# Kernel tuning notes

Measured on AMD Instinct MI355X. Metric: run time of the kernel, lower is better.

## Reference

```python
import jax, jax.numpy as jnp
import numpy as np

B, T, D = 8, 2048, 256
EPS_NORM = 1e-8
EPS_LN = 1e-6


def _layer_norm(x, gamma, beta):
    mu = jnp.mean(x, axis=-1, keepdims=True)
    var = jnp.var(x, axis=-1, keepdims=True)
    return (x - mu) * jax.lax.rsqrt(var + EPS_LN) * gamma + beta


def setup_inputs() -> dict:
    key = jax.random.key(0)
    ks = jax.random.split(key, 8)
    xav = np.sqrt(2.0 / (D + D)).astype(np.float32)  # xavier_uniform-ish scale
    a_fea = jax.random.normal(ks[0], (B, T, D), jnp.float32)
    v_fea = jax.random.normal(ks[1], (B, T, D), jnp.float32)
    Wv1 = jax.random.normal(ks[2], (D, D), jnp.float32) * xav
    Wv2 = jax.random.normal(ks[3], (D, D), jnp.float32) * xav
    Wa1 = jax.random.normal(ks[4], (D, D), jnp.float32) * xav
    Wa2 = jax.random.normal(ks[5], (D, D), jnp.float32) * xav
    ln_gamma = jnp.ones((D,), jnp.float32)
    ln_beta = jnp.zeros((D,), jnp.float32)
    thr_val = jnp.asarray(0.099, jnp.float32)
    return {"a_fea": a_fea, "v_fea": v_fea, "Wv1": Wv1, "Wv2": Wv2,
            "Wa1": Wa1, "Wa2": Wa2, "ln_gamma": ln_gamma, "ln_beta": ln_beta,
            "thr_val": thr_val}


def reference(a_fea, v_fea, Wv1, Wv2, Wa1, Wa2, ln_gamma, ln_beta, thr_val):
    # Dropout is identity in eval mode. Linear(bias=False): x @ W^T; here W is [in, out].
    v_b1 = jax.nn.relu(jnp.einsum('btd,dh->bth', v_fea, Wv1))
    v_b2 = jax.nn.relu(jnp.einsum('btd,dh->bth', v_fea, Wv2))
    a_b1 = jax.nn.relu(jnp.einsum('btd,dh->bth', a_fea, Wa1))
    a_b2 = jax.nn.relu(jnp.einsum('btd,dh->bth', a_fea, Wa2))

    scale = 1.0 / jnp.sqrt(jnp.asarray(v_b2.shape[2], jnp.float32))
    # relu-gated cross-modal scores [B, Tv, Ta]
    beta = jax.nn.relu(jnp.einsum('bvh,bah->bva', v_b2, a_b1) * scale)

    # v->a: normalize over audio axis, threshold-sparsify
    beta_va = beta / (jnp.sum(beta, axis=-1, keepdims=True) + EPS_NORM)
    gamma_va = jnp.where(beta_va > thr_val, beta_va, 0.0)
    # a->v: transpose of UN-normalized beta (faithful to source ordering)
    beta_av = jnp.swapaxes(beta, 1, 2)
    beta_av = beta_av / (jnp.sum(beta_av, axis=-1, keepdims=True) + EPS_NORM)
    gamma_av = jnp.where(beta_av > thr_val, beta_av, 0.0)

    a_pos = jnp.einsum('bva,bah->bvh', gamma_va, a_b2)
    v_pos = jnp.einsum('bav,bvh->bah', gamma_av, v_b1)

    v_psp = _layer_norm(v_fea + a_pos, ln_gamma, ln_beta)
    a_psp = _layer_norm(a_fea + v_pos, ln_gamma, ln_beta)
    return (v_psp + a_psp) * 0.5
```

## Files before the change

kernel.cpp:

```cpp
#include <hip/hip_runtime.h>
#include <stdint.h>

#define B_ 8
#define T_ 2048
#define D_ 256
#define M_ (B_*T_)

typedef uint16_t u16;
typedef __attribute__((ext_vector_type(8))) short   short8;
typedef __attribute__((ext_vector_type(8))) __bf16  bf16x8;
typedef __attribute__((ext_vector_type(4))) float   f32x4;
typedef __attribute__((ext_vector_type(4))) uint32_t u32x4;

__device__ __forceinline__ float bf2f(u16 b){
    union { uint32_t u; float f; } v; v.u = ((uint32_t)b) << 16; return v.f;
}
__device__ __forceinline__ u16 f2bf(float f){
    union { float f; uint32_t u; } v; v.f = f;
    uint32_t u = v.u;
    u += 0x7FFFu + ((u >> 16) & 1u);
    return (u16)(u >> 16);
}

typedef __attribute__((address_space(1))) void gvoid;
typedef __attribute__((address_space(3))) void lvoid;
__device__ __forceinline__ void gl16(const void* g, void* l){
    __builtin_amdgcn_global_load_lds((gvoid*)(unsigned long long)g, (lvoid*)l, 16, 0, 0);
}

__global__ void k_detect(const uint32_t* g, int* flag){
    *flag = (g[0] == 0x3F803F80u) ? 0 : 1;
}

struct WtArgs { const void* w[4]; u16* wt[4]; const int* flag; };

__global__ __launch_bounds__(256) void k_wt(WtArgs a){
    int f32in = *a.flag;
    int m = blockIdx.y;
    int d = blockIdx.x;
    int h = threadIdx.x;
    float val;
    if (f32in) val = ((const float*)a.w[m])[(size_t)d * D_ + h];
    else       val = bf2f(((const u16*)a.w[m])[(size_t)d * D_ + h]);
    a.wt[m][(size_t)h * D_ + d] = f2bf(val);
}

struct ProjArgs { const void* x[4]; const u16* wt[4]; u16* y[4]; u16* yt[4]; const int* flag; };

__global__ __launch_bounds__(256) void k_proj(ProjArgs args){
    __shared__ __align__(16) u16 Xs[128][72];
    __shared__ __align__(16) u16 Ws[128][72];
    int f32in = *args.flag;
    int id = blockIdx.x;
    int m  = id & 127;
    int vh = id >> 7;
    int hh = vh & 1;
    int v  = vh >> 1;
    const u16* Wt = args.wt[v];
    u16*       Y  = args.y[v];
    u16*       YT = args.yt[v];
    int t_base = m * 128;
    int h_base = hh * 128;

    int tid  = threadIdx.x;
    int w    = tid >> 6, lane = tid & 63;
    int wm   = w >> 1, wn = w & 1;
    int l15  = lane & 15, quad = lane >> 4;

    int srow = tid >> 1;
    int shalf = tid & 1;

    f32x4 acc[4][4];
#pragma unroll
    for (int i = 0; i < 4; ++i)
#pragma unroll
        for (int j = 0; j < 4; ++j) acc[i][j] = (f32x4){0.f,0.f,0.f,0.f};

    float4 pXf[8];
    short8 pXb[4];
    short8 pW[4];

    const float* Xf = (const float*)args.x[v] + (size_t)(t_base + srow)*D_ + shalf*32;
    const u16*   Xb = (const u16*)args.x[v]   + (size_t)(t_base + srow)*D_ + shalf*32;
    const u16*   Wp = Wt + (size_t)(h_base + srow)*D_ + shalf*32;

    if (f32in){
#pragma unroll
        for (int i = 0; i < 8; ++i) pXf[i] = *(const float4*)(Xf + i*4);
    } else {
#pragma unroll
        for (int i = 0; i < 4; ++i) pXb[i] = *(const short8*)(Xb + i*8);
    }
#pragma unroll
    for (int i = 0; i < 4; ++i) pW[i] = *(const short8*)(Wp + i*8);

    for (int k0 = 0; k0 < D_; k0 += 64){
        __syncthreads();
        if (f32in){
#pragma unroll
            for (int i = 0; i < 4; ++i){
                float4 a0 = pXf[i*2], a1 = pXf[i*2+1];
                short8 o;
                o[0]=(short)f2bf(a0.x); o[1]=(short)f2bf(a0.y); o[2]=(short)f2bf(a0.z); o[3]=(short)f2bf(a0.w);
                o[4]=(short)f2bf(a1.x); o[5]=(short)f2bf(a1.y); o[6]=(short)f2bf(a1.z); o[7]=(short)f2bf(a1.w);
                *(short8*)(&Xs[srow][shalf*32 + i*8]) = o;
            }
        } else {
#pragma unroll
            for (int i = 0; i < 4; ++i) *(short8*)(&Xs[srow][shalf*32 + i*8]) = pXb[i];
        }
#pragma unroll
        for (int i = 0; i < 4; ++i) *(short8*)(&Ws[srow][shalf*32 + i*8]) = pW[i];

        int kn = k0 + 64;
        if (kn < D_){
            if (f32in){
#pragma unroll
                for (int i = 0; i < 8; ++i) pXf[i] = *(const float4*)(Xf + kn + i*4);
            } else {
#pragma unroll
                for (int i = 0; i < 4; ++i) pXb[i] = *(const short8*)(Xb + kn + i*8);
            }
#pragma unroll
            for (int i = 0; i < 4; ++i) pW[i] = *(const short8*)(Wp + kn + i*8);
        }
        __syncthreads();

#pragma unroll
        for (int kc = 0; kc < 2; ++kc){
            bf16x8 af[4], bf[4];
#pragma unroll
            for (int i = 0; i < 4; ++i){
                af[i] = __builtin_bit_cast(bf16x8,
                         *(const short8*)(&Xs[wm*64 + i*16 + l15][kc*32 + quad*8]));
                bf[i] = __builtin_bit_cast(bf16x8,
                         *(const short8*)(&Ws[wn*64 + i*16 + l15][kc*32 + quad*8]));
            }
#pragma unroll
            for (int mt = 0; mt < 4; ++mt)
#pragma unroll
                for (int nt = 0; nt < 4; ++nt)
                    acc[mt][nt] = __builtin_amdgcn_mfma_f32_16x16x32_bf16(
                                      af[mt], bf[nt], acc[mt][nt], 0, 0, 0);
        }
    }

    int v0 = t_base + wm*64;
    int h0 = h_base + wn*64;
#pragma unroll
    for (int mt = 0; mt < 4; ++mt){
#pragma unroll
        for (int nt = 0; nt < 4; ++nt){
            int col = h0 + nt*16 + l15;
            u16 q[4];
#pragma unroll
            for (int r = 0; r < 4; ++r){
                float s = acc[mt][nt][r]; s = s > 0.f ? s : 0.f;
                q[r] = f2bf(s);
            }
            if (Y){
#pragma unroll
                for (int r = 0; r < 4; ++r)
                    Y[(size_t)(v0 + mt*16 + quad*4 + r)*D_ + col] = q[r];
            }
            if (YT){
                int row0 = v0 + mt*16 + quad*4;
                int bb   = row0 >> 11;
                int tl   = row0 & (T_-1);
                uint2 pk;
                pk.x = (uint32_t)q[0] | ((uint32_t)q[1] << 16);
                pk.y = (uint32_t)q[2] | ((uint32_t)q[3] << 16);
                *(uint2*)(YT + ((size_t)(bb*D_ + col))*T_ + tl) = pk;
            }
        }
    }
}

__global__ __launch_bounds__(256) void k_score(const u16* vb2, const u16* ab1,
                                               u16* beta, u16* betaT,
                                               float* rowsum, float* colsum){
    __shared__ __align__(16) u16 SMEM[2*128*72];
    u16 (*As)[72] = (u16(*)[72])(SMEM);
    u16 (*Bs)[72] = (u16(*)[72])(SMEM + 128*72);
    int id = blockIdx.x;
    int b  = id & 7;
    int t  = id >> 3;
    int mb = t & 15;
    int ab = t >> 4;
    int tid  = threadIdx.x;
    int w    = tid >> 6, lane = tid & 63;
    int wm   = w >> 1, wn = w & 1;
    int l15  = lane & 15, quad = lane >> 4;
    int v_base = mb*128;
    int a_base = ab*128;

    const u16* vb = vb2 + (size_t)b*T_*D_;
    const u16* an = ab1 + (size_t)b*T_*D_;
    u16*   bbp = beta  + (size_t)b*T_*T_;
    u16*   bbt = betaT + (size_t)b*T_*T_;
    float* rs  = rowsum + b*T_;
    float* cs  = colsum + b*T_;

    int kk = tid & 7;
    int mm = tid >> 3;

    f32x4 acc[4][4];
#pragma unroll
    for (int i = 0; i < 4; ++i)
#pragma unroll
        for (int j = 0; j < 4; ++j) acc[i][j] = (f32x4){0.f,0.f,0.f,0.f};

    short8 pA[4], pB[4];
#pragma unroll
    for (int i = 0; i < 4; ++i){
        int row = mm + i*32;
        pA[i] = *(const short8*)(vb + (size_t)(v_base + row)*D_ + kk*8);
        pB[i] = *(const short8*)(an + (size_t)(a_base + row)*D_ + kk*8);
    }

    for (int k0 = 0; k0 < D_; k0 += 64){
        __syncthreads();
#pragma unroll
        for (int i = 0; i < 4; ++i){
            int row = mm + i*32;
            *(short8*)(&As[row][kk*8]) = pA[i];
            *(short8*)(&Bs[row][kk*8]) = pB[i];
        }
        int kn = k0 + 64;
        if (kn < D_){
#pragma unroll
            for (int i = 0; i < 4; ++i){
                int row = mm + i*32;
                pA[i] = *(const short8*)(vb + (size_t)(v_base + row)*D_ + kn + kk*8);
                pB[i] = *(const short8*)(an + (size_t)(a_base + row)*D_ + kn + kk*8);
            }
        }
        __syncthreads();

#pragma unroll
        for (int kc = 0; kc < 2; ++kc){
            bf16x8 af[4], bf[4];
#pragma unroll
            for (int i = 0; i < 4; ++i){
                af[i] = __builtin_bit_cast(bf16x8,
                         *(const short8*)(&As[wm*64 + i*16 + l15][kc*32 + quad*8]));
                bf[i] = __builtin_bit_cast(bf16x8,
                         *(const short8*)(&Bs[wn*64 + i*16 + l15][kc*32 + quad*8]));
            }
#pragma unroll
            for (int mt = 0; mt < 4; ++mt)
#pragma unroll
                for (int nt = 0; nt < 4; ++nt)
                    acc[mt][nt] = __builtin_amdgcn_mfma_f32_16x16x32_bf16(
                                      af[mt], bf[nt], acc[mt][nt], 0, 0, 0);
        }
    }

    int v0 = v_base + wm*64;
    int a0 = a_base + wn*64;
    float rsum[4][4];
    float csum[4] = {0.f,0.f,0.f,0.f};
    uint2 qq[4][4];
#pragma unroll
    for (int mt = 0; mt < 4; ++mt)
#pragma unroll
        for (int r = 0; r < 4; ++r) rsum[mt][r] = 0.f;

#pragma unroll
    for (int mt = 0; mt < 4; ++mt){
#pragma unroll
        for (int nt = 0; nt < 4; ++nt){
            u16 q[4];
#pragma unroll
            for (int r = 0; r < 4; ++r){
                float s = acc[mt][nt][r] * 0.0625f;
                s = s > 0.f ? s : 0.f;
                q[r] = f2bf(s);
                bbp[(size_t)(v0 + mt*16 + quad*4 + r)*T_ + a0 + nt*16 + l15] = q[r];
                rsum[mt][r] += s;
                csum[nt]    += s;
            }
            qq[mt][nt].x = (uint32_t)q[0] | ((uint32_t)q[1] << 16);
            qq[mt][nt].y = (uint32_t)q[2] | ((uint32_t)q[3] << 16);
        }
    }
#pragma unroll
    for (int mt = 0; mt < 4; ++mt){
#pragma unroll
        for (int r = 0; r < 4; ++r){
            float v = rsum[mt][r];
            v += __shfl_xor(v, 1);
            v += __shfl_xor(v, 2);
            v += __shfl_xor(v, 4);
            v += __shfl_xor(v, 8);
            if (l15 == 0) atomicAdd(&rs[v0 + mt*16 + quad*4 + r], v);
        }
    }
#pragma unroll
    for (int nt = 0; nt < 4; ++nt){
        float v = csum[nt];
        v += __shfl_xor(v, 16);
        v += __shfl_xor(v, 32);
        if (quad == 0) atomicAdd(&cs[a0 + nt*16 + l15], v);
    }

    u16* tile = SMEM;
    __syncthreads();
#pragma unroll
    for (int mt = 0; mt < 4; ++mt){
#pragma unroll
        for (int nt = 0; nt < 4; ++nt){
            int va = wm*64 + mt*16 + quad*4;
            int aa = wn*64 + nt*16 + l15;
            *(uint2*)(tile + (size_t)aa*136 + va) = qq[mt][nt];
        }
    }
    __syncthreads();
#pragma unroll
    for (int it = 0; it < 8; ++it){
        int flat = it*256 + tid;
        int aa = flat >> 4, ch = flat & 15;
        u32x4 d = *(const u32x4*)(tile + (size_t)aa*136 + ch*8);
        *(u32x4*)(bbt + (size_t)(a_base + aa)*T_ + v_base + ch*8) = d;
    }
}

__global__ __launch_bounds__(256) void k_pos4(const u16* beta, const u16* betaT,
                                              const u16* ab2T, const u16* vb1T,
                                              const float* rowsum, const float* colsum,
                                              const void* thrp, const int* flag,
                                              u16* apos, u16* vpos){
    __shared__ __align__(16) u16 SL[2][2][128*64];
    int f32in = *flag;
    int id = blockIdx.x;
    int nb    = id & 1;
    int mb    = (id >> 1) & 15;
    int b     = (id >> 5) & 7;
    int which = id >> 8;

    const u16* A   = (which ? betaT : beta) + (size_t)b*T_*T_;
    const u16* Bt  = (which ? vb1T  : ab2T) + (size_t)b*T_*D_;
    const float* nrm = (which ? colsum : rowsum) + b*T_;
    u16* outb = (which ? vpos : apos) + (size_t)b*T_*D_;

    float thr = f32in ? *(const float*)thrp : bf2f(*(const u16*)thrp);

    int tid = threadIdx.x;
    int w = tid >> 6, lane = tid & 63;
    int l15 = lane & 15, quad = lane >> 4;

    int m0 = mb * 128;
    int h0 = nb * 128;

    int srow = w*32 + (lane >> 3);
    int schk = (lane & 7) ^ ((lane >> 3) & 7);
    const u16* gA = A  + (size_t)(m0 + srow)*T_ + schk*8;
    const u16* gB = Bt + (size_t)(h0 + srow)*T_ + schk*8;

    uint32_t thp[2];
#pragma unroll
    for (int i = 0; i < 2; ++i){
        float ts = thr * (nrm[m0 + w*32 + i*16 + l15] + 1e-8f);
        union { float f; uint32_t u; } cv; cv.f = ts;
        uint32_t th16 = cv.u >> 16;
        thp[i] = th16 * 0x10001u;
    }

    f32x4 acc[2][8];
#pragma unroll
    for (int i = 0; i < 2; ++i)
#pragma unroll
        for (int j = 0; j < 8; ++j) acc[i][j] = (f32x4){0.f,0.f,0.f,0.f};

#pragma unroll
    for (int c = 0; c < 4; ++c){
        gl16(gA + (size_t)c*8*T_, &SL[0][0][(w*32 + c*8)*64]);
        gl16(gB + (size_t)c*8*T_, &SL[0][1][(w*32 + c*8)*64]);
    }

    int q = 0;
    for (int k0 = 0; k0 < T_; k0 += 64){
        __syncthreads();
        int kn = k0 + 64;
        if (kn < T_){
#pragma unroll
            for (int c = 0; c < 4; ++c){
                gl16(gA + (size_t)c*8*T_ + kn, &SL[q^1][0][(w*32 + c*8)*64]);
                gl16(gB + (size_t)c*8*T_ + kn, &SL[q^1][1][(w*32 + c*8)*64]);
            }
        }
        const u16* Asb = &SL[q][0][0];
        const u16* Bsb = &SL[q][1][0];
#pragma unroll
        for (int kc = 0; kc < 2; ++kc){
            int sw = ((kc*4 + quad) ^ (l15 & 7)) * 8;
            bf16x8 af[2];
#pragma unroll
            for (int i = 0; i < 2; ++i){
                u32x4 ra = *(const u32x4*)(Asb + (size_t)(w*32 + i*16 + l15)*64 + sw);
                u32x4 om;
#pragma unroll
                for (int jd = 0; jd < 4; ++jd){
                    uint32_t t, m;
                    asm("v_pk_sub_u16 %0, %1, %2" : "=v"(t) : "v"(thp[i]), "v"(ra[jd]));
                    asm("v_pk_ashrrev_i16 %0, 15, %1" : "=v"(m) : "v"(t));
                    om[jd] = ra[jd] & m;
                }
                af[i] = __builtin_bit_cast(bf16x8, om);
            }
#pragma unroll
            for (int nt = 0; nt < 8; ++nt){
                bf16x8 bfr = __builtin_bit_cast(bf16x8,
                              *(const short8*)(Bsb + (size_t)(nt*16 + l15)*64 + sw));
                acc[0][nt] = __builtin_amdgcn_mfma_f32_16x16x32_bf16(
                                  af[0], bfr, acc[0][nt], 0, 0, 0);
                acc[1][nt] = __builtin_amdgcn_mfma_f32_16x16x32_bf16(
                                  af[1], bfr, acc[1][nt], 0, 0, 0);
            }
        }
        q ^= 1;
    }

#pragma unroll
    for (int i = 0; i < 2; ++i){
#pragma unroll
        for (int r = 0; r < 4; ++r){
            int row = m0 + w*32 + i*16 + quad*4 + r;
            float iv = 1.f / (nrm[row] + 1e-8f);
#pragma unroll
            for (int nt = 0; nt < 8; ++nt)
                outb[(size_t)row*D_ + h0 + nt*16 + l15] =
                    f2bf(acc[i][nt][r] * iv);
        }
    }
}

__global__ __launch_bounds__(256) void k_ln(const void* vfea, const void* afea,
                                            const u16* apos, const u16* vpos,
                                            const void* g, const void* lnb,
                                            const int* flag, void* out){
    int f32in = *flag;
    int row = blockIdx.x;
    int c   = threadIdx.x;
    size_t idx = (size_t)row * D_ + c;
    float xv = f32in ? ((const float*)vfea)[idx] : bf2f(((const u16*)vfea)[idx]);
    float xa = f32in ? ((const float*)afea)[idx] : bf2f(((const u16*)afea)[idx]);
    float x1 = xv + bf2f(apos[idx]);
    float x2 = xa + bf2f(vpos[idx]);
    float s1 = x1, q1 = x1*x1, s2 = x2, q2 = x2*x2;
#pragma unroll
    for (int off = 1; off < 64; off <<= 1){
        s1 += __shfl_xor(s1, off);
        q1 += __shfl_xor(q1, off);
        s2 += __shfl_xor(s2, off);
        q2 += __shfl_xor(q2, off);
    }
    __shared__ float red[4][4];
    int wave = threadIdx.x >> 6;
    if ((threadIdx.x & 63) == 0){
        red[0][wave] = s1; red[1][wave] = q1; red[2][wave] = s2; red[3][wave] = q2;
    }
    __syncthreads();
    s1 = red[0][0]+red[0][1]+red[0][2]+red[0][3];
    q1 = red[1][0]+red[1][1]+red[1][2]+red[1][3];
    s2 = red[2][0]+red[2][1]+red[2][2]+red[2][3];
    q2 = red[3][0]+red[3][1]+red[3][2]+red[3][3];
    const float invD = 1.f / (float)D_;
    float mu1 = s1*invD, mu2 = s2*invD;
    float var1 = q1*invD - mu1*mu1;
    float var2 = q2*invD - mu2*mu2;
    float rs1 = rsqrtf(var1 + 1e-6f);
    float rs2 = rsqrtf(var2 + 1e-6f);
    float gg = f32in ? ((const float*)g)[c]   : bf2f(((const u16*)g)[c]);
    float bv = f32in ? ((const float*)lnb)[c] : bf2f(((const u16*)lnb)[c]);
    float y = 0.5f * (((x1-mu1)*rs1)*gg + bv + ((x2-mu2)*rs2)*gg + bv);
    if (f32in) ((float*)out)[idx] = y;
    else       ((u16*)out)[idx]   = f2bf(y);
}

extern "C" void kernel_launch(void* const* d_in, const int* in_sizes, int n_in,
                              void* d_out, int out_size, void* d_ws, size_t ws_size,
                              hipStream_t stream){
    (void)in_sizes; (void)n_in; (void)out_size; (void)ws_size;
    const void* a_fea = d_in[0];
    const void* v_fea = d_in[1];
    const void* Wv1   = d_in[2];
    const void* Wv2   = d_in[3];
    const void* Wa1   = d_in[4];
    const void* Wa2   = d_in[5];
    const void* lng   = d_in[6];
    const void* lnb   = d_in[7];
    const void* thrp  = d_in[8];
    char* ws = (char*)d_ws;

    const size_t ACT  = (size_t)M_ * D_ * 2;
    const size_t BETA = (size_t)B_ * T_ * T_ * 2;
    size_t off_wt    = 0;
    size_t off_vb2   = 524288;
    size_t off_ab1   = off_vb2  + ACT;
    size_t off_vb1T  = off_ab1  + ACT;
    size_t off_ab2T  = off_vb1T + ACT;
    size_t off_beta  = off_ab2T + ACT;
    size_t off_betaT = off_beta  + BETA;
    size_t off_rsum  = off_betaT + BETA;
    size_t off_csum  = off_rsum + (size_t)B_*T_*4;
    size_t off_apos  = off_csum + (size_t)B_*T_*4;
    size_t off_vpos  = off_apos + ACT;
    size_t off_flag  = off_vpos + ACT;

    u16* wt0   = (u16*)(ws + off_wt);
    u16* vb2   = (u16*)(ws + off_vb2);
    u16* ab1   = (u16*)(ws + off_ab1);
    u16* vb1T  = (u16*)(ws + off_vb1T);
    u16* ab2T  = (u16*)(ws + off_ab2T);
    u16* beta  = (u16*)(ws + off_beta);
    u16* betaT = (u16*)(ws + off_betaT);
    float* rowsum = (float*)(ws + off_rsum);
    float* colsum = (float*)(ws + off_csum);
    u16*   apos   = (u16*)(ws + off_apos);
    u16*   vpos   = (u16*)(ws + off_vpos);
    int*   flag   = (int*)(ws + off_flag);

    hipMemsetAsync(ws + off_rsum, 0, 2 * (size_t)B_ * T_ * sizeof(float), stream);

    k_detect<<<1, 1, 0, stream>>>((const uint32_t*)lng, flag);

    WtArgs wa;
    wa.w[0] = Wv1; wa.w[1] = Wv2; wa.w[2] = Wa1; wa.w[3] = Wa2;
    for (int i = 0; i < 4; ++i) wa.wt[i] = wt0 + (size_t)i * D_ * D_;
    wa.flag = flag;
    k_wt<<<dim3(256,4), 256, 0, stream>>>(wa);

    ProjArgs pa;
    pa.x[0] = v_fea; pa.x[1] = v_fea; pa.x[2] = a_fea; pa.x[3] = a_fea;
    for (int i = 0; i < 4; ++i) pa.wt[i] = wa.wt[i];
    pa.y[0] = nullptr; pa.y[1] = vb2; pa.y[2] = ab1; pa.y[3] = nullptr;
    pa.yt[0] = vb1T;   pa.yt[1] = nullptr; pa.yt[2] = nullptr; pa.yt[3] = ab2T;
    pa.flag = flag;
    k_proj<<<4*2*(M_/128), 256, 0, stream>>>(pa);

    k_score<<<8*16*16, 256, 0, stream>>>(vb2, ab1, beta, betaT, rowsum, colsum);

    k_pos4<<<512, 256, 0, stream>>>(beta, betaT, ab2T, vb1T, rowsum, colsum,
                                    thrp, flag, apos, vpos);

    k_ln<<<M_, 256, 0, stream>>>(v_fea, a_fea, apos, vpos, lng, lnb, flag, d_out);
}
```

Baseline: 246.7 us.

## Restructure pos GEMM to 512 threads with register-direct A loads

The sparse-gated attention-times-value kernel now runs 8 waves per block in a 4x2 wave grid, each wave owning a 32x64 output tile. The A operand (beta rows) is loaded straight from global memory into registers and prefetched one step ahead, instead of being staged through shared memory, which halves LDS use and removes the LDS reads for A. Block IDs are also remapped so that neighbouring blocks run on different batches or chunks, changing the order of L2 and XCD traffic. The cost is uncoalesced per-lane global reads for A and more register pressure under the 4-blocks launch bound.

```diff
diff --git a/kernel.cpp b/kernel.cpp
--- a/kernel.cpp
+++ b/kernel.cpp
@@ -325,14 +325,15 @@
     }
 }
 
-__global__ __launch_bounds__(256) void k_pos4(const u16* beta, const u16* betaT,
+__global__ __launch_bounds__(512, 4) void k_pos5(const u16* beta, const u16* betaT,
                                               const u16* ab2T, const u16* vb1T,
                                               const float* rowsum, const float* colsum,
                                               const void* thrp, const int* flag,
                                               u16* apos, u16* vpos){
-    __shared__ __align__(16) u16 SL[2][2][128*64];
+    __shared__ __align__(16) u16 SL[2][128*64];
     int f32in = *flag;
-    int id = blockIdx.x;
+    int s  = blockIdx.x;
+    int id = (s & 7) * 64 + (s >> 3);
     int nb    = id & 1;
     int mb    = (id >> 1) & 15;
     int b     = (id >> 5) & 7;
@@ -347,57 +348,66 @@
 
     int tid = threadIdx.x;
     int w = tid >> 6, lane = tid & 63;
+    int wm = w >> 1, wn = w & 1;
     int l15 = lane & 15, quad = lane >> 4;
 
     int m0 = mb * 128;
     int h0 = nb * 128;
 
-    int srow = w*32 + (lane >> 3);
     int schk = (lane & 7) ^ ((lane >> 3) & 7);
-    const u16* gA = A  + (size_t)(m0 + srow)*T_ + schk*8;
-    const u16* gB = Bt + (size_t)(h0 + srow)*T_ + schk*8;
+    const u16* gB = Bt + (size_t)(h0 + w*8 + (lane >> 3))*T_ + schk*8;
+
+    const u16* gA = A + (size_t)(m0 + wm*32 + l15)*T_;
 
     uint32_t thp[2];
 #pragma unroll
     for (int i = 0; i < 2; ++i){
-        float ts = thr * (nrm[m0 + w*32 + i*16 + l15] + 1e-8f);
+        float ts = thr * (nrm[m0 + wm*32 + i*16 + l15] + 1e-8f);
         union { float f; uint32_t u; } cv; cv.f = ts;
         uint32_t th16 = cv.u >> 16;
         thp[i] = th16 * 0x10001u;
     }
 
-    f32x4 acc[2][8];
+    f32x4 acc[2][4];
 #pragma unroll
     for (int i = 0; i < 2; ++i)
 #pragma unroll
-        for (int j = 0; j < 8; ++j) acc[i][j] = (f32x4){0.f,0.f,0.f,0.f};
-
-#pragma unroll
-    for (int c = 0; c < 4; ++c){
-        gl16(gA + (size_t)c*8*T_, &SL[0][0][(w*32 + c*8)*64]);
-        gl16(gB + (size_t)c*8*T_, &SL[0][1][(w*32 + c*8)*64]);
-    }
+        for (int j = 0; j < 4; ++j) acc[i][j] = (f32x4){0.f,0.f,0.f,0.f};
+
+#pragma unroll
+    for (int c = 0; c < 2; ++c)
+        gl16(gB + (size_t)c*64*T_, &SL[0][(c*64 + w*8)*64]);
+    short8 pa[4];
+#pragma unroll
+    for (int i = 0; i < 2; ++i)
+#pragma unroll
+        for (int kc = 0; kc < 2; ++kc)
+            pa[i*2+kc] = *(const short8*)(gA + (size_t)i*16*T_ + kc*32 + quad*8);
 
     int q = 0;
     for (int k0 = 0; k0 < T_; k0 += 64){
         __syncthreads();
         int kn = k0 + 64;
+        short8 ac[4];
+#pragma unroll
+        for (int i = 0; i < 4; ++i) ac[i] = pa[i];
         if (kn < T_){
 #pragma unroll
-            for (int c = 0; c < 4; ++c){
-                gl16(gA + (size_t)c*8*T_ + kn, &SL[q^1][0][(w*32 + c*8)*64]);
-                gl16(gB + (size_t)c*8*T_ + kn, &SL[q^1][1][(w*32 + c*8)*64]);
-            }
-        }
-        const u16* Asb = &SL[q][0][0];
-        const u16* Bsb = &SL[q][1][0];
-#pragma unroll
-        for (int kc = 0; kc < 2; ++kc){
-            int sw = ((kc*4 + quad) ^ (l15 & 7)) * 8;
-            bf16x8 af[2];
-#pragma unroll
-            for (int i = 0; i < 2; ++i){
-                u32x4 ra = *(const u32x4*)(Asb + (size_t)(w*32 + i*16 + l15)*64 + sw);
+            for (int c = 0; c < 2; ++c)
+                gl16(gB + (size_t)c*64*T_ + kn, &SL[q^1][(c*64 + w*8)*64]);
+#pragma unroll
+            for (int i = 0; i < 2; ++i)
+#pragma unroll
+                for (int kc = 0; kc < 2; ++kc)
+                    pa[i*2+kc] = *(const short8*)(gA + (size_t)i*16*T_ + kn + kc*32 + quad*8);
+        }
+
+        bf16x8 af[4];
+#pragma unroll
+        for (int i = 0; i < 2; ++i){
+#pragma unroll
+            for (int kc = 0; kc < 2; ++kc){
+                u32x4 ra = __builtin_bit_cast(u32x4, ac[i*2+kc]);
                 u32x4 om;
 #pragma unroll
                 for (int jd = 0; jd < 4; ++jd){
@@ -406,16 +416,22 @@
                     asm("v_pk_ashrrev_i16 %0, 15, %1" : "=v"(m) : "v"(t));
                     om[jd] = ra[jd] & m;
                 }
-                af[i] = __builtin_bit_cast(bf16x8, om);
-            }
-#pragma unroll
-            for (int nt = 0; nt < 8; ++nt){
+                af[i*2+kc] = __builtin_bit_cast(bf16x8, om);
+            }
+        }
+
+        const u16* Bsb = &SL[q][0];
+#pragma unroll
+        for (int kc = 0; kc < 2; ++kc){
+            int sw = ((kc*4 + quad) ^ (l15 & 7)) * 8;
+#pragma unroll
+            for (int nt = 0; nt < 4; ++nt){
                 bf16x8 bfr = __builtin_bit_cast(bf16x8,
-                              *(const short8*)(Bsb + (size_t)(nt*16 + l15)*64 + sw));
+                              *(const short8*)(Bsb + (size_t)(wn*64 + nt*16 + l15)*64 + sw));
                 acc[0][nt] = __builtin_amdgcn_mfma_f32_16x16x32_bf16(
-                                  af[0], bfr, acc[0][nt], 0, 0, 0);
+                                  af[0*2+kc], bfr, acc[0][nt], 0, 0, 0);
                 acc[1][nt] = __builtin_amdgcn_mfma_f32_16x16x32_bf16(
-                                  af[1], bfr, acc[1][nt], 0, 0, 0);
+                                  af[1*2+kc], bfr, acc[1][nt], 0, 0, 0);
             }
         }
         q ^= 1;
@@ -425,11 +441,11 @@
     for (int i = 0; i < 2; ++i){
 #pragma unroll
         for (int r = 0; r < 4; ++r){
-            int row = m0 + w*32 + i*16 + quad*4 + r;
+            int row = m0 + wm*32 + i*16 + quad*4 + r;
             float iv = 1.f / (nrm[row] + 1e-8f);
 #pragma unroll
-            for (int nt = 0; nt < 8; ++nt)
-                outb[(size_t)row*D_ + h0 + nt*16 + l15] =
+            for (int nt = 0; nt < 4; ++nt)
+                outb[(size_t)row*D_ + h0 + wn*64 + nt*16 + l15] =
                     f2bf(acc[i][nt][r] * iv);
         }
     }
@@ -541,7 +557,7 @@
 
     k_score<<<8*16*16, 256, 0, stream>>>(vb2, ab1, beta, betaT, rowsum, colsum);
 
-    k_pos4<<<512, 256, 0, stream>>>(beta, betaT, ab2T, vb1T, rowsum, colsum,
+    k_pos5<<<512, 512, 0, stream>>>(beta, betaT, ab2T, vb1T, rowsum, colsum,
                                     thrp, flag, apos, vpos);
 
     k_ln<<<M_, 256, 0, stream>>>(v_fea, a_fea, apos, vpos, lng, lnb, flag, d_out);
```

Result: slower. 264.8 us (+7.3%).
